# Kernel tuning notes

Hardware: AMD Instinct MI355X
Metric: run time of the kernel (lower is better)

Reference implementation:

```python
import jax, jax.numpy as jnp
import numpy as np

S, A, F, L, NCONV = 16, 512, 64, 12, 3


def setup_inputs() -> dict:
    key = jax.random.key(0)
    k1, k2, k3, k4 = jax.random.split(key, 4)
    node = jax.random.normal(k1, (S, A, F), dtype=jnp.float32)
    conn = jax.random.uniform(k2, (S, A, A, L), dtype=jnp.float32)
    bond = jax.random.normal(k3, (S, A, L, 2), dtype=jnp.float32)
    # filters.data.normal_() * (1/in_depth/1000) per ChemConv.__init__
    filters = jax.random.normal(k4, (NCONV, F, L, F + 2), dtype=jnp.float32) / (F * 1000.0)
    return {
        "node_property_tensor": node,
        "connectivity_tensor": conn,
        "bond_property_tensor": bond,
        "filters": filters,
    }


def _chemconv(x, conn, bond, w):
    # x: (S,A,F); conn: (S,A,A,L); bond: (S,A,L,2); w: (O,L,F+2)
    # gather neighbor features: bmm of (S,A,L,A) x (S,A,F) -> (S,A,L,F)
    ncv = jnp.einsum('sakl,skf->salf', conn, x)
    combined = jnp.concatenate([ncv, bond], axis=-1)  # (S,A,L,F+2)
    # elementwise-mul + double-sum == contraction over (L, F+2)
    return jnp.einsum('salc,olc->sao', combined, w)  # (S,A,O)


def reference(node_property_tensor, connectivity_tensor, bond_property_tensor, filters):
    out = node_property_tensor
    for i in range(filters.shape[0]):
        w = filters[i]  # same conv layer applied twice per residual pair
        out = jax.nn.relu(_chemconv(out, connectivity_tensor, bond_property_tensor, w))
        out = _chemconv(out, connectivity_tensor, bond_property_tensor, w)
        out = out + node_property_tensor  # residual to block input
        out = jax.nn.relu(out)
    return out
```

## Files before the change

### kernel.cpp

```cpp
#include <hip/hip_runtime.h>


typedef __attribute__((ext_vector_type(8))) short bf16x8;
typedef __attribute__((ext_vector_type(4))) float f32x4;
typedef unsigned short u16;
typedef unsigned int u32;
typedef unsigned char u8;
typedef long i64t;

#define YSCALE 16384.0f
#define YINV   (1.0f / 16384.0f)

__device__ __forceinline__ u16 f2bf(float f) {
  union { float f; u32 u; } x; x.f = f;
  u32 r = x.u + 0x7fffu + ((x.u >> 16) & 1u);
  return (u16)(r >> 16);
}

__device__ __forceinline__ u32 fp8pk4(float a, float b, float c, float d) {
  u32 w = __builtin_amdgcn_cvt_pk_fp8_f32(a, b, 0u, false);
  return __builtin_amdgcn_cvt_pk_fp8_f32(c, d, w, true);
}
__device__ __forceinline__ u32 fp8one(float v) {
  return __builtin_amdgcn_cvt_pk_fp8_f32(v, v, 0u, false) & 0xffu;
}

__device__ __forceinline__ void gload16(const void* g, void* l) {
  __builtin_amdgcn_global_load_lds((const __attribute__((address_space(1))) u32*)g,
                                   (__attribute__((address_space(3))) u32*)l, 16, 0, 0);
}

__global__ __launch_bounds__(256) void k_prep(const float* __restrict__ filters,
                                              const float* __restrict__ bond,
                                              u16* __restrict__ wA,
                                              float* __restrict__ bW) {
  const int bid = blockIdx.x, tid = threadIdx.x;
  if (bid < 576) {
    int t = bid * 256 + tid;
    int i = t / 49152;
    int rem = t - i * 49152;
    int row = rem >> 6, f = rem & 63;
    int l = row >> 6, o = row & 63;
    wA[t] = f2bf(filters[((size_t)((i * 64 + o) * 12 + l)) * 66 + f]);
  } else {
    __shared__ float wb[4608];
    __shared__ float lb[16 * 24];
    const int sa0 = (bid - 576) * 16;
    for (int idx = tid; idx < 4608; idx += 256) {
      int i = idx / 1536, rem = idx - i * 1536;
      int o = rem / 24, lj = rem - o * 24;
      wb[idx] = filters[((size_t)((i * 64 + o) * 12 + (lj >> 1))) * 66 + 64 + (lj & 1)];
    }
    for (int t = tid; t < 384; t += 256)
      lb[t] = bond[(size_t)sa0 * 24 + t];
    __syncthreads();
#pragma unroll
    for (int it = 0; it < 12; ++it) {
      int idx = it * 256 + tid;
      int sl = idx / 192, rem = idx - sl * 192;
      int i = rem >> 6, o = rem & 63;
      float acc = 0.f;
#pragma unroll
      for (int lj = 0; lj < 24; ++lj)
        acc += lb[sl * 24 + lj] * wb[i * 1536 + o * 24 + lj];
      bW[(size_t)i * 524288 + (size_t)(sa0 + sl) * 64 + o] = acc;
    }
  }
}

__global__ __launch_bounds__(256) void k_yT(const float* __restrict__ node,
                                            const float* __restrict__ pOut,
                                            const float* __restrict__ bias,
                                            const u16* __restrict__ wAf,
                                            u8* __restrict__ yT,
                                            int mode, int addNode) {
  const int s = blockIdx.y, k0 = blockIdx.x * 32;
  __shared__ u16 xld[32 * 64];
  __shared__ u16 Z[12 * 64 * 36];
  const int tid = threadIdx.x, lane = tid & 63, wid = tid >> 6;
  const int r = lane & 15, g = lane >> 4;

  {
    const int row = tid >> 3, f0 = (tid & 7) * 8;
    const size_t e = ((size_t)(s * 512) + k0 + row) * 64 + f0;
    float v[8];
    if (mode == 0) {
      float4 a = *(const float4*)&node[e], b = *(const float4*)&node[e + 4];
      v[0] = a.x; v[1] = a.y; v[2] = a.z; v[3] = a.w;
      v[4] = b.x; v[5] = b.y; v[6] = b.z; v[7] = b.w;
    } else {
      float4 sa = {0, 0, 0, 0}, sb = {0, 0, 0, 0};
#pragma unroll
      for (int q = 0; q < 4; ++q) {
        float4 a = *(const float4*)&pOut[(size_t)q * 524288 + e];
        float4 b = *(const float4*)&pOut[(size_t)q * 524288 + e + 4];
        sa.x += a.x; sa.y += a.y; sa.z += a.z; sa.w += a.w;
        sb.x += b.x; sb.y += b.y; sb.z += b.z; sb.w += b.w;
      }
      float4 ba = *(const float4*)&bias[e], bb = *(const float4*)&bias[e + 4];
      sa.x = sa.x * YINV + ba.x; sa.y = sa.y * YINV + ba.y;
      sa.z = sa.z * YINV + ba.z; sa.w = sa.w * YINV + ba.w;
      sb.x = sb.x * YINV + bb.x; sb.y = sb.y * YINV + bb.y;
      sb.z = sb.z * YINV + bb.z; sb.w = sb.w * YINV + bb.w;
      if (addNode) {
        float4 na = *(const float4*)&node[e], nb = *(const float4*)&node[e + 4];
        sa.x += na.x; sa.y += na.y; sa.z += na.z; sa.w += na.w;
        sb.x += nb.x; sb.y += nb.y; sb.z += nb.z; sb.w += nb.w;
      }
      v[0] = fmaxf(sa.x, 0.f); v[1] = fmaxf(sa.y, 0.f);
      v[2] = fmaxf(sa.z, 0.f); v[3] = fmaxf(sa.w, 0.f);
      v[4] = fmaxf(sb.x, 0.f); v[5] = fmaxf(sb.y, 0.f);
      v[6] = fmaxf(sb.z, 0.f); v[7] = fmaxf(sb.w, 0.f);
    }
    ushort4 h0, h1;
    h0.x = f2bf(v[0]); h0.y = f2bf(v[1]); h0.z = f2bf(v[2]); h0.w = f2bf(v[3]);
    h1.x = f2bf(v[4]); h1.y = f2bf(v[5]); h1.z = f2bf(v[6]); h1.w = f2bf(v[7]);
    const int slot = (f0 >> 3) ^ (row & 7);
    *(ushort4*)&xld[row * 64 + slot * 8] = h0;
    *(ushort4*)&xld[row * 64 + slot * 8 + 4] = h1;
  }
  __syncthreads();

#pragma unroll
  for (int lw = 0; lw < 3; ++lw) {
    const int l = wid * 3 + lw;
    f32x4 acc[4][2] = {};
#pragma unroll
    for (int ks = 0; ks < 2; ++ks) {
      bf16x8 bv[2];
#pragma unroll
      for (int kt = 0; kt < 2; ++kt) {
        const int kk = kt * 16 + r;
        bv[kt] = *(const bf16x8*)&xld[kk * 64 + (((ks * 4 + g) ^ (kk & 7)) << 3)];
      }
#pragma unroll
      for (int ot = 0; ot < 4; ++ot) {
        bf16x8 av = *(const bf16x8*)&wAf[(size_t)(l * 64 + ot * 16 + r) * 64 + ks * 32 + g * 8];
#pragma unroll
        for (int kt = 0; kt < 2; ++kt)
          acc[ot][kt] = __builtin_amdgcn_mfma_f32_16x16x32_bf16(av, bv[kt], acc[ot][kt], 0, 0, 0);
      }
    }
#pragma unroll
    for (int ot = 0; ot < 4; ++ot)
#pragma unroll
      for (int kt = 0; kt < 2; ++kt)
#pragma unroll
        for (int r2 = 0; r2 < 4; ++r2) {
          int o = ot * 16 + g * 4 + r2, k = kt * 16 + r;
          Z[l * 2304 + o * 36 + k] = (u16)fp8one(acc[ot][kt][r2] * YSCALE);
        }
  }
  __syncthreads();
  u8* yb = yT + (size_t)s * 393216;
#pragma unroll
  for (int it = 0; it < 8; ++it) {
    int idx = it * 256 + tid;
    int o = idx >> 5, k = idx & 31;
    u32 b[12];
#pragma unroll
    for (int l = 0; l < 12; ++l) b[l] = (u32)(Z[l * 2304 + o * 36 + k] & 0xffu);
    u32* dst = (u32*)&yb[(size_t)o * 6144 + (size_t)(k0 + k) * 12];
    dst[0] = b[0] | (b[1] << 8) | (b[2] << 16) | (b[3] << 24);
    dst[1] = b[4] | (b[5] << 8) | (b[6] << 16) | (b[7] << 24);
    dst[2] = b[8] | (b[9] << 8) | (b[10] << 16) | (b[11] << 24);
  }
}

template <int CVT>
__global__ __launch_bounds__(512, 2) void k_stageB(const float* __restrict__ connF,
                                                   u8* __restrict__ connQ,
                                                   const u8* __restrict__ yT,
                                                   float* __restrict__ pOut) {
  const int b = blockIdx.x;
  const int s = (b & 7) * 2 + ((b >> 3) & 1);
  const int mt = (b >> 4) & 7, kq = b >> 7;
  const int row0 = mt * 64, k0 = kq * 1536;
  const u8* Ab = connQ + (size_t)(s * 512 + row0) * 6144 + k0;
  const u8* Bb = yT + (size_t)(s * 64) * 6144 + k0;
  __shared__ __align__(16) u8 lds[3 * 2 * 4096];
  const int tid = threadIdx.x, lane = tid & 63, wid = tid >> 6;
  const int r = lane & 15, g = lane >> 4;
  const int wr = wid & 3, wc = wid >> 2;
  const int isA = wid < 4;
  const int wseg = (isA ? wid : wid - 4) * 16;
  const int lrow = lane >> 2, lslot = lane & 3;
  f32x4 acc[2] = {};

#define ASTAGE(T, NB)                                                           \
  {                                                                             \
    const int row = wseg + lrow;                                                \
    const int slot = lslot ^ ((row ^ (row >> 2)) & 3);                          \
    gload16(Ab + (size_t)row * 6144 + (size_t)(T) * 64 + slot * 16,             \
            &lds[((NB) * 2 + 0) * 4096 + wseg * 64]);                           \
  }
#define BSTAGE(T, NB)                                                           \
  {                                                                             \
    const int row = wseg + lrow;                                                \
    const int slot = lslot ^ ((row ^ (row >> 2)) & 3);                          \
    gload16(Bb + (size_t)row * 6144 + (size_t)(T) * 64 + slot * 16,             \
            &lds[((NB) * 2 + 1) * 4096 + wseg * 64]);                           \
  }
#define COMPUTE(NB)                                                             \
  {                                                                             \
    const u8* bufA = &lds[((NB) * 2 + 0) * 4096];                               \
    const u8* bufB = &lds[((NB) * 2 + 1) * 4096];                               \
    const int arow = wr * 16 + r;                                               \
    const int ax = (arow ^ (arow >> 2)) & 3;                                    \
    _Pragma("unroll")                                                           \
    for (int ks = 0; ks < 2; ++ks) {                                            \
      i64t av = *(const i64t*)&bufA[arow * 64 + (((ks * 2 + (g >> 1)) ^ ax) << 4) + ((g & 1) << 3)]; \
      _Pragma("unroll")                                                         \
      for (int c = 0; c < 2; ++c) {                                             \
        const int col = wc * 32 + c * 16 + r;                                   \
        const int bx = (col ^ (col >> 2)) & 3;                                  \
        i64t bv = *(const i64t*)&bufB[col * 64 + (((ks * 2 + (g >> 1)) ^ bx) << 4) + ((g & 1) << 3)]; \
        acc[c] = __builtin_amdgcn_mfma_f32_16x16x32_fp8_fp8(av, bv, acc[c], 0, 0, 0); \
      }                                                                         \
    }                                                                           \
  }

  if constexpr (!CVT) {
    const int side = isA ? 0 : 1;
    const u8* sbase = isA ? Ab : Bb;
#define STAGE(T, NB)                                                            \
  {                                                                             \
    const int row = wseg + lrow;                                                \
    const int slot = lslot ^ ((row ^ (row >> 2)) & 3);                          \
    gload16(sbase + (size_t)row * 6144 + (size_t)(T) * 64 + slot * 16,          \
            &lds[((NB) * 2 + side) * 4096 + wseg * 64]);                        \
  }
    STAGE(0, 0);
    STAGE(1, 1);
    int nb = 0;
    for (int t = 0; t < 24; ++t) {
      if (t < 23) { asm volatile("s_waitcnt vmcnt(1)" ::: "memory"); }
      else        { asm volatile("s_waitcnt vmcnt(0)" ::: "memory"); }
      __builtin_amdgcn_s_barrier();
      if (t + 2 < 24) {
        int nb2 = nb + 2; if (nb2 >= 3) nb2 -= 3;
        STAGE(t + 2, nb2);
      }
      COMPUTE(nb);
      if (++nb >= 3) nb -= 3;
    }
#undef STAGE
  } else {
    const int grow = s * 512 + row0 + wseg + lrow;
    const float* afp = connF + (size_t)grow * 6144 + k0 + lslot * 16;
    u8* aqp = connQ + (size_t)grow * 6144 + k0 + lslot * 16;
    float4 pa0[4], pa1[4];
#define ALOADF(PA, T)                                                           \
    { const float* p = afp + (size_t)(T) * 64;                                  \
      PA[0] = *(const float4*)(p + 0);  PA[1] = *(const float4*)(p + 4);        \
      PA[2] = *(const float4*)(p + 8);  PA[3] = *(const float4*)(p + 12); }
#define ACVTW(PA, T, NB)                                                        \
    { uint4 q;                                                                  \
      q.x = fp8pk4(PA[0].x, PA[0].y, PA[0].z, PA[0].w);                         \
      q.y = fp8pk4(PA[1].x, PA[1].y, PA[1].z, PA[1].w);                         \
      q.z = fp8pk4(PA[2].x, PA[2].y, PA[2].z, PA[2].w);                         \
      q.w = fp8pk4(PA[3].x, PA[3].y, PA[3].z, PA[3].w);                         \
      const int row = wseg + lrow;                                              \
      const int dslot = lslot ^ ((row ^ (row >> 2)) & 3);                       \
      *(uint4*)&lds[((NB) * 2 + 0) * 4096 + row * 64 + dslot * 16] = q;         \
      *(uint4*)(aqp + (size_t)(T) * 64) = q; }

    if (isA) { ALOADF(pa0, 0); ALOADF(pa1, 1); ACVTW(pa0, 0, 0); ALOADF(pa0, 2); }
    else     { BSTAGE(0, 0); BSTAGE(1, 1); }
#pragma unroll
    for (int t = 0; t < 24; ++t) {
      if (isA) {
        asm volatile("s_waitcnt lgkmcnt(0)" ::: "memory");
      } else {
        if (t < 23) asm volatile("s_waitcnt vmcnt(1)" ::: "memory");
        else        asm volatile("s_waitcnt vmcnt(0)" ::: "memory");
      }
      __builtin_amdgcn_s_barrier();
      if (isA) {
        if (t < 23) {
          if ((t + 1) & 1) { ACVTW(pa1, t + 1, (t + 1) % 3); }
          else             { ACVTW(pa0, t + 1, (t + 1) % 3); }
          if (t + 3 < 24) {
            if ((t + 3) & 1) { ALOADF(pa1, t + 3); }
            else             { ALOADF(pa0, t + 3); }
          }
        }
      } else {
        if (t + 2 < 24) BSTAGE(t + 2, (t + 2) % 3);
      }
      COMPUTE(t % 3);
    }
#undef ALOADF
#undef ACVTW
  }
#undef ASTAGE
#undef BSTAGE
#undef COMPUTE

  float* po = pOut + (size_t)kq * 524288 + ((size_t)(s * 512) + row0) * 64;
#pragma unroll
  for (int c = 0; c < 2; ++c)
#pragma unroll
    for (int r2 = 0; r2 < 4; ++r2) {
      int m = wr * 16 + g * 4 + r2;
      int o = wc * 32 + c * 16 + r;
      po[m * 64 + o] = acc[c][r2];
    }
}

__global__ __launch_bounds__(256) void k_finalLast(const float* __restrict__ pOut,
                                                   const float* __restrict__ bW,
                                                   const float* __restrict__ node,
                                                   float* __restrict__ outF) {
  size_t e = ((size_t)blockIdx.x * 256 + threadIdx.x) * 4;
  float4 sv = {0, 0, 0, 0};
#pragma unroll
  for (int q = 0; q < 4; ++q) {
    float4 a = *(const float4*)&pOut[(size_t)q * 524288 + e];
    sv.x += a.x; sv.y += a.y; sv.z += a.z; sv.w += a.w;
  }
  float4 bw = *(const float4*)&bW[e];
  float4 nd = *(const float4*)&node[e];
  sv.x = fmaxf(sv.x * YINV + bw.x + nd.x, 0.f);
  sv.y = fmaxf(sv.y * YINV + bw.y + nd.y, 0.f);
  sv.z = fmaxf(sv.z * YINV + bw.z + nd.z, 0.f);
  sv.w = fmaxf(sv.w * YINV + bw.w + nd.w, 0.f);
  *(float4*)&outF[e] = sv;
}

__global__ __launch_bounds__(256) void k_fb_conv(const float* __restrict__ x,
                                                 const float* __restrict__ conn,
                                                 const float* __restrict__ bond,
                                                 const float* __restrict__ filt,
                                                 const float* __restrict__ node,
                                                 float* __restrict__ out, int addNode) {
  const int s = blockIdx.y, a = blockIdx.x;
  const int t = threadIdx.x;
  const int f = t & 63, lg = t >> 6;
  __shared__ float ncv[12 * 64];
  __shared__ float red[4][64];
  const float* cb = conn + ((size_t)(s * 512 + a)) * 6144;
  const float* xb = x + (size_t)s * 32768;
  float a0 = 0.f, a1 = 0.f, a2 = 0.f;
  for (int k = 0; k < 512; ++k) {
    float xv = xb[k * 64 + f];
    const float* cr = cb + k * 12 + lg * 3;
    a0 += cr[0] * xv; a1 += cr[1] * xv; a2 += cr[2] * xv;
  }
  ncv[(lg * 3 + 0) * 64 + f] = a0;
  ncv[(lg * 3 + 1) * 64 + f] = a1;
  ncv[(lg * 3 + 2) * 64 + f] = a2;
  __syncthreads();
  float p = 0.f;
  for (int l = lg * 3; l < lg * 3 + 3; ++l) {
    const float* wr = filt + ((size_t)(f * 12 + l)) * 66;
    float q = 0.f;
    for (int f2 = 0; f2 < 64; ++f2) q += ncv[l * 64 + f2] * wr[f2];
    q += bond[((size_t)(s * 512 + a) * 12 + l) * 2 + 0] * wr[64];
    q += bond[((size_t)(s * 512 + a) * 12 + l) * 2 + 1] * wr[65];
    p += q;
  }
  red[lg][f] = p;
  __syncthreads();
  if (t < 64) {
    float v = red[0][t] + red[1][t] + red[2][t] + red[3][t];
    if (addNode) v += node[((size_t)(s * 512 + a)) * 64 + t];
    out[((size_t)(s * 512 + a)) * 64 + t] = fmaxf(v, 0.f);
  }
}

extern "C" void kernel_launch(void* const* d_in, const int* in_sizes, int n_in,
                              void* d_out, int out_size, void* d_ws, size_t ws_size,
                              hipStream_t stream) {
  (void)in_sizes; (void)n_in; (void)out_size;
  const float* node    = (const float*)d_in[0];
  const float* conn    = (const float*)d_in[1];
  const float* bond    = (const float*)d_in[2];
  const float* filters = (const float*)d_in[3];
  float* outF = (float*)d_out;

  const size_t OFF_CONNQ = 0;
  const size_t OFF_YT    = 50331648;
  const size_t OFF_WA    = 56623104;
  const size_t OFF_BW    = 56918016;
  const size_t OFF_POUT  = 63209472;
  const size_t WS_NEED   = 71598080;

  if (ws_size >= WS_NEED) {
    unsigned char* ws = (unsigned char*)d_ws;
    u8*  connQ = (u8*)(ws + OFF_CONNQ);
    u8*  yT    = (u8*)(ws + OFF_YT);
    u16* wA    = (u16*)(ws + OFF_WA);
    float* bW  = (float*)(ws + OFF_BW);
    float* pO  = (float*)(ws + OFF_POUT);

    k_prep<<<dim3(1088), dim3(256), 0, stream>>>(filters, bond, wA, bW);
    k_yT<<<dim3(16, 16), dim3(256), 0, stream>>>(node, pO, bW, wA, yT, 0, 0);
    for (int j = 0; j < 6; ++j) {
      if (j == 0)
        k_stageB<1><<<dim3(512), dim3(512), 0, stream>>>(conn, connQ, yT, pO);
      else
        k_stageB<0><<<dim3(512), dim3(512), 0, stream>>>(conn, connQ, yT, pO);
      if (j < 5) {
        k_yT<<<dim3(16, 16), dim3(256), 0, stream>>>(node, pO,
                                                     bW + (size_t)(j >> 1) * 524288,
                                                     wA + (size_t)((j + 1) >> 1) * 49152,
                                                     yT, 1, j & 1);
      } else {
        k_finalLast<<<dim3(512), dim3(256), 0, stream>>>(pO, bW + (size_t)2 * 524288,
                                                         node, outF);
      }
    }
  } else {
    float* buf = (float*)d_ws;
    const float* xc = node;
    for (int j = 0; j < 6; ++j) {
      int i = j >> 1;
      float* dst = (j & 1) ? outF : buf;
      k_fb_conv<<<dim3(512, 16), dim3(256), 0, stream>>>(xc, conn, bond,
                                                         filters + (size_t)i * 50688,
                                                         node, dst, j & 1);
      xc = dst;
    }
  }
}
```

Baseline: 176.3 us.

## Remove prep kernel, fold bond-bias into first stageB, convert filters inline

```diff
diff --git a/kernel.cpp b/kernel.cpp
--- a/kernel.cpp
+++ b/kernel.cpp
@@ -30,48 +30,17 @@
                                    (__attribute__((address_space(3))) u32*)l, 16, 0, 0);
 }
 
-__global__ __launch_bounds__(256) void k_prep(const float* __restrict__ filters,
-                                              const float* __restrict__ bond,
-                                              u16* __restrict__ wA,
-                                              float* __restrict__ bW) {
-  const int bid = blockIdx.x, tid = threadIdx.x;
-  if (bid < 576) {
-    int t = bid * 256 + tid;
-    int i = t / 49152;
-    int rem = t - i * 49152;
-    int row = rem >> 6, f = rem & 63;
-    int l = row >> 6, o = row & 63;
-    wA[t] = f2bf(filters[((size_t)((i * 64 + o) * 12 + l)) * 66 + f]);
-  } else {
-    __shared__ float wb[4608];
-    __shared__ float lb[16 * 24];
-    const int sa0 = (bid - 576) * 16;
-    for (int idx = tid; idx < 4608; idx += 256) {
-      int i = idx / 1536, rem = idx - i * 1536;
-      int o = rem / 24, lj = rem - o * 24;
-      wb[idx] = filters[((size_t)((i * 64 + o) * 12 + (lj >> 1))) * 66 + 64 + (lj & 1)];
-    }
-    for (int t = tid; t < 384; t += 256)
-      lb[t] = bond[(size_t)sa0 * 24 + t];
-    __syncthreads();
-#pragma unroll
-    for (int it = 0; it < 12; ++it) {
-      int idx = it * 256 + tid;
-      int sl = idx / 192, rem = idx - sl * 192;
-      int i = rem >> 6, o = rem & 63;
-      float acc = 0.f;
-#pragma unroll
-      for (int lj = 0; lj < 24; ++lj)
-        acc += lb[sl * 24 + lj] * wb[i * 1536 + o * 24 + lj];
-      bW[(size_t)i * 524288 + (size_t)(sa0 + sl) * 64 + o] = acc;
-    }
-  }
+__device__ __forceinline__ bf16x8 cvt8bf(const float* p) {
+  union { u16 u[8]; bf16x8 v; } t;
+#pragma unroll
+  for (int e = 0; e < 8; ++e) t.u[e] = f2bf(p[e]);
+  return t.v;
 }
 
 __global__ __launch_bounds__(256) void k_yT(const float* __restrict__ node,
                                             const float* __restrict__ pOut,
                                             const float* __restrict__ bias,
-                                            const u16* __restrict__ wAf,
+                                            const float* __restrict__ filt,
                                             u8* __restrict__ yT,
                                             int mode, int addNode) {
   const int s = blockIdx.y, k0 = blockIdx.x * 32;
@@ -135,7 +104,8 @@
       }
 #pragma unroll
       for (int ot = 0; ot < 4; ++ot) {
-        bf16x8 av = *(const bf16x8*)&wAf[(size_t)(l * 64 + ot * 16 + r) * 64 + ks * 32 + g * 8];
+        const int o = ot * 16 + r;
+        bf16x8 av = cvt8bf(filt + ((size_t)o * 12 + l) * 66 + ks * 32 + g * 8);
 #pragma unroll
         for (int kt = 0; kt < 2; ++kt)
           acc[ot][kt] = __builtin_amdgcn_mfma_f32_16x16x32_bf16(av, bv[kt], acc[ot][kt], 0, 0, 0);
@@ -171,36 +141,52 @@
 __global__ __launch_bounds__(512, 2) void k_stageB(const float* __restrict__ connF,
                                                    u8* __restrict__ connQ,
                                                    const u8* __restrict__ yT,
-                                                   float* __restrict__ pOut) {
+                                                   float* __restrict__ pOut,
+                                                   const float* __restrict__ bond,
+                                                   const float* __restrict__ filters,
+                                                   float* __restrict__ bW) {
+  __shared__ __align__(16) u8 lds[3 * 2 * 4096];
   const int b = blockIdx.x;
+  const int tid = threadIdx.x;
+
+  if constexpr (CVT) {
+    if (b >= 512) {
+      float* wb = (float*)lds;
+      float* lb = wb + 4608;
+      const int sa0 = (b - 512) * 16;
+      for (int idx = tid; idx < 4608; idx += 512) {
+        int i = idx / 1536, rem = idx - i * 1536;
+        int o = rem / 24, lj = rem - o * 24;
+        wb[idx] = filters[((size_t)((i * 64 + o) * 12 + (lj >> 1))) * 66 + 64 + (lj & 1)];
+      }
+      for (int t = tid; t < 384; t += 512)
+        lb[t] = bond[(size_t)sa0 * 24 + t];
+      __syncthreads();
+#pragma unroll
+      for (int it = 0; it < 6; ++it) {
+        int idx = it * 512 + tid;
+        int sl = idx / 192, rem = idx - sl * 192;
+        int i = rem >> 6, o = rem & 63;
+        float acc = 0.f;
+#pragma unroll
+        for (int lj = 0; lj < 24; ++lj)
+          acc += lb[sl * 24 + lj] * wb[i * 1536 + o * 24 + lj];
+        bW[(size_t)i * 524288 + (size_t)(sa0 + sl) * 64 + o] = acc;
+      }
+      return;
+    }
+  }
+
   const int s = (b & 7) * 2 + ((b >> 3) & 1);
   const int mt = (b >> 4) & 7, kq = b >> 7;
   const int row0 = mt * 64, k0 = kq * 1536;
   const u8* Ab = connQ + (size_t)(s * 512 + row0) * 6144 + k0;
   const u8* Bb = yT + (size_t)(s * 64) * 6144 + k0;
-  __shared__ __align__(16) u8 lds[3 * 2 * 4096];
-  const int tid = threadIdx.x, lane = tid & 63, wid = tid >> 6;
+  const int lane = tid & 63, wid = tid >> 6;
   const int r = lane & 15, g = lane >> 4;
   const int wr = wid & 3, wc = wid >> 2;
-  const int isA = wid < 4;
-  const int wseg = (isA ? wid : wid - 4) * 16;
-  const int lrow = lane >> 2, lslot = lane & 3;
   f32x4 acc[2] = {};
 
-#define ASTAGE(T, NB)                                                           \
-  {                                                                             \
-    const int row = wseg + lrow;                                                \
-    const int slot = lslot ^ ((row ^ (row >> 2)) & 3);                          \
-    gload16(Ab + (size_t)row * 6144 + (size_t)(T) * 64 + slot * 16,             \
-            &lds[((NB) * 2 + 0) * 4096 + wseg * 64]);                           \
-  }
-#define BSTAGE(T, NB)                                                           \
-  {                                                                             \
-    const int row = wseg + lrow;                                                \
-    const int slot = lslot ^ ((row ^ (row >> 2)) & 3);                          \
-    gload16(Bb + (size_t)row * 6144 + (size_t)(T) * 64 + slot * 16,             \
-            &lds[((NB) * 2 + 1) * 4096 + wseg * 64]);                           \
-  }
 #define COMPUTE(NB)                                                             \
   {                                                                             \
     const u8* bufA = &lds[((NB) * 2 + 0) * 4096];                               \
@@ -221,6 +207,9 @@
   }
 
   if constexpr (!CVT) {
+    const int isA = wid < 4;
+    const int wseg = (isA ? wid : wid - 4) * 16;
+    const int lrow = lane >> 2, lslot = lane & 3;
     const int side = isA ? 0 : 1;
     const u8* sbase = isA ? Ab : Bb;
 #define STAGE(T, NB)                                                            \
@@ -246,55 +235,62 @@
     }
 #undef STAGE
   } else {
-    const int grow = s * 512 + row0 + wseg + lrow;
-    const float* afp = connF + (size_t)grow * 6144 + k0 + lslot * 16;
-    u8* aqp = connQ + (size_t)grow * 6144 + k0 + lslot * 16;
+    const int halfA = (lane < 32);
+    const int lrow8 = wid * 8 + ((lane & 31) >> 2);
+    const int sg = lane & 3;
+    const int dslot = sg ^ ((lrow8 ^ (lrow8 >> 2)) & 3);
+    const float* aF = connF + (size_t)(s * 512 + row0 + lrow8) * 6144 + k0 + sg * 16;
+    u8* aQ = connQ + (size_t)(s * 512 + row0 + lrow8) * 6144 + k0 + sg * 16;
+    const u8* bF = yT + (size_t)(s * 64 + lrow8) * 6144 + k0 + sg * 16;
+    const int ldsoffA = lrow8 * 64 + dslot * 16;
     float4 pa0[4], pa1[4];
-#define ALOADF(PA, T)                                                           \
-    { const float* p = afp + (size_t)(T) * 64;                                  \
-      PA[0] = *(const float4*)(p + 0);  PA[1] = *(const float4*)(p + 4);        \
-      PA[2] = *(const float4*)(p + 8);  PA[3] = *(const float4*)(p + 12); }
-#define ACVTW(PA, T, NB)                                                        \
-    { uint4 q;                                                                  \
-      q.x = fp8pk4(PA[0].x, PA[0].y, PA[0].z, PA[0].w);                         \
-      q.y = fp8pk4(PA[1].x, PA[1].y, PA[1].z, PA[1].w);                         \
-      q.z = fp8pk4(PA[2].x, PA[2].y, PA[2].z, PA[2].w);                         \
-      q.w = fp8pk4(PA[3].x, PA[3].y, PA[3].z, PA[3].w);                         \
-      const int row = wseg + lrow;                                              \
-      const int dslot = lslot ^ ((row ^ (row >> 2)) & 3);                       \
-      *(uint4*)&lds[((NB) * 2 + 0) * 4096 + row * 64 + dslot * 16] = q;         \
-      *(uint4*)(aqp + (size_t)(T) * 64) = q; }
-
-    if (isA) { ALOADF(pa0, 0); ALOADF(pa1, 1); ACVTW(pa0, 0, 0); ALOADF(pa0, 2); }
-    else     { BSTAGE(0, 0); BSTAGE(1, 1); }
+    uint4 pb0, pb1;
+
+#define LOADS(T, P)                                                             \
+    {                                                                           \
+      if (halfA) {                                                              \
+        const float* p = aF + (size_t)(T) * 64;                                 \
+        pa##P[0] = *(const float4*)(p + 0);  pa##P[1] = *(const float4*)(p + 4);\
+        pa##P[2] = *(const float4*)(p + 8);  pa##P[3] = *(const float4*)(p + 12);\
+      } else {                                                                  \
+        pb##P = *(const uint4*)(bF + (size_t)(T) * 64);                         \
+      }                                                                         \
+    }
+#define WRITES(T, NB, P)                                                        \
+    {                                                                           \
+      if (halfA) {                                                              \
+        uint4 q;                                                                \
+        q.x = fp8pk4(pa##P[0].x, pa##P[0].y, pa##P[0].z, pa##P[0].w);           \
+        q.y = fp8pk4(pa##P[1].x, pa##P[1].y, pa##P[1].z, pa##P[1].w);           \
+        q.z = fp8pk4(pa##P[2].x, pa##P[2].y, pa##P[2].z, pa##P[2].w);           \
+        q.w = fp8pk4(pa##P[3].x, pa##P[3].y, pa##P[3].z, pa##P[3].w);           \
+        *(uint4*)&lds[(NB) * 8192 + ldsoffA] = q;                               \
+        *(uint4*)(aQ + (size_t)(T) * 64) = q;                                   \
+      } else {                                                                  \
+        *(uint4*)&lds[(NB) * 8192 + 4096 + ldsoffA] = pb##P;                    \
+      }                                                                         \
+    }
+
+    LOADS(0, 0); LOADS(1, 1);
+    WRITES(0, 0, 0);
+    asm volatile("s_waitcnt lgkmcnt(0)" ::: "memory");
+    __builtin_amdgcn_s_barrier();
 #pragma unroll
     for (int t = 0; t < 24; ++t) {
-      if (isA) {
-        asm volatile("s_waitcnt lgkmcnt(0)" ::: "memory");
-      } else {
-        if (t < 23) asm volatile("s_waitcnt vmcnt(1)" ::: "memory");
-        else        asm volatile("s_waitcnt vmcnt(0)" ::: "memory");
-      }
+      if (t + 2 < 24) {
+        if (t & 1) { LOADS(t + 2, 1); } else { LOADS(t + 2, 0); }
+      }
+      if (t + 1 < 24) {
+        const int nbw = (t + 1) % 3;
+        if ((t + 1) & 1) { WRITES(t + 1, nbw, 1); } else { WRITES(t + 1, nbw, 0); }
+      }
+      COMPUTE(t % 3);
+      asm volatile("s_waitcnt lgkmcnt(0)" ::: "memory");
       __builtin_amdgcn_s_barrier();
-      if (isA) {
-        if (t < 23) {
-          if ((t + 1) & 1) { ACVTW(pa1, t + 1, (t + 1) % 3); }
-          else             { ACVTW(pa0, t + 1, (t + 1) % 3); }
-          if (t + 3 < 24) {
-            if ((t + 3) & 1) { ALOADF(pa1, t + 3); }
-            else             { ALOADF(pa0, t + 3); }
-          }
-        }
-      } else {
-        if (t + 2 < 24) BSTAGE(t + 2, (t + 2) % 3);
-      }
-      COMPUTE(t % 3);
-    }
-#undef ALOADF
-#undef ACVTW
-  }
-#undef ASTAGE
-#undef BSTAGE
+    }
+#undef LOADS
+#undef WRITES
+  }
 #undef COMPUTE
 
   float* po = pOut + (size_t)kq * 524288 + ((size_t)(s * 512) + row0) * 64;
@@ -381,31 +377,30 @@
 
   const size_t OFF_CONNQ = 0;
   const size_t OFF_YT    = 50331648;
-  const size_t OFF_WA    = 56623104;
-  const size_t OFF_BW    = 56918016;
-  const size_t OFF_POUT  = 63209472;
-  const size_t WS_NEED   = 71598080;
+  const size_t OFF_BW    = 56623104;
+  const size_t OFF_POUT  = 62914560;
+  const size_t WS_NEED   = 71303168;
 
   if (ws_size >= WS_NEED) {
     unsigned char* ws = (unsigned char*)d_ws;
     u8*  connQ = (u8*)(ws + OFF_CONNQ);
-    u8*  yT    = (u8*)(ws + OFF_YT);
-    u16* wA    = (u16*)(ws + OFF_WA);
+    u8*  yTb   = (u8*)(ws + OFF_YT);
     float* bW  = (float*)(ws + OFF_BW);
     float* pO  = (float*)(ws + OFF_POUT);
 
-    k_prep<<<dim3(1088), dim3(256), 0, stream>>>(filters, bond, wA, bW);
-    k_yT<<<dim3(16, 16), dim3(256), 0, stream>>>(node, pO, bW, wA, yT, 0, 0);
+    k_yT<<<dim3(16, 16), dim3(256), 0, stream>>>(node, pO, bW, filters, yTb, 0, 0);
     for (int j = 0; j < 6; ++j) {
       if (j == 0)
-        k_stageB<1><<<dim3(512), dim3(512), 0, stream>>>(conn, connQ, yT, pO);
+        k_stageB<1><<<dim3(1024), dim3(512), 0, stream>>>(conn, connQ, yTb, pO,
+                                                          bond, filters, bW);
       else
-        k_stageB<0><<<dim3(512), dim3(512), 0, stream>>>(conn, connQ, yT, pO);
+        k_stageB<0><<<dim3(512), dim3(512), 0, stream>>>(conn, connQ, yTb, pO,
+                                                         bond, filters, bW);
       if (j < 5) {
         k_yT<<<dim3(16, 16), dim3(256), 0, stream>>>(node, pO,
                                                      bW + (size_t)(j >> 1) * 524288,
-                                                     wA + (size_t)((j + 1) >> 1) * 49152,
-                                                     yT, 1, j & 1);
+                                                     filters + (size_t)((j + 1) >> 1) * 50688,
+                                                     yTb, 1, j & 1);
       } else {
         k_finalLast<<<dim3(512), dim3(256), 0, stream>>>(pO, bW + (size_t)2 * 524288,
                                                          node, outF);
```

Result: slower. 185.6 us (+5.3%).
